# Kernel tuning notes

Measured on AMD Instinct MI355X. Metric: run time of the kernel, lower is better.

## Reference

```python
import jax, jax.numpy as jnp
import numpy as np

B, T, S, H, E, V, M = 64, 59, 32, 512, 300, 34004, 1024  # batch, dec steps, enc len, hidden, embed, vocab, enc dim (bi)


def setup_inputs() -> dict:
    key = jax.random.key(0)
    ks = jax.random.split(key, 14)
    w = lambda k, sh, sc=0.05: jax.random.normal(k, sh, jnp.float32) * sc
    return dict(
        dec_input=jax.random.randint(ks[0], (B, T), 0, V),
        enc_output=w(ks[1], (B, S, M), 1.0),
        enc_h=w(ks[2], (B, H), 1.0),
        enc_c=w(ks[3], (B, H), 1.0),
        embedding=w(ks[4], (V, E)),
        Wx=w(ks[5], (E + H, 4 * H)),   # LSTM input kernel (input = [emb; prev_attention])
        Uh=w(ks[6], (H, 4 * H)),       # LSTM recurrent kernel
        b=jnp.zeros((4 * H,), jnp.float32),
        Wm=w(ks[7], (M, H)),           # Bahdanau memory layer
        Wq=w(ks[8], (H, H)),           # Bahdanau query layer
        v=w(ks[9], (H,)),              # Bahdanau attention vector
        Wa=w(ks[10], (H + M, H)),      # attention_layer (Dense, no bias)
        Wf=w(ks[11], (H, V)),          # output projection to vocab
        bf=jnp.zeros((V,), jnp.float32),
    )


def reference(dec_input, enc_output, enc_h, enc_c, embedding, Wx, Uh, b, Wm, Wq, v, Wa, Wf, bf):
    # Precompute attention keys once: [B,S,H]
    keys = jnp.einsum('bsm,mh->bsh', enc_output, Wm)
    emb = embedding[dec_input]            # [B,T,E] teacher-forced inputs
    emb_t = jnp.swapaxes(emb, 0, 1)       # [T,B,E]

    def step(carry, x_t):
        h, c, attn = carry
        x = jnp.concatenate([x_t, attn], axis=-1)          # [B,E+H]
        z = x @ Wx + h @ Uh + b                            # [B,4H]
        i, f, g, o = jnp.split(z, 4, axis=-1)              # keras gate order i,f,c,o
        c2 = jax.nn.sigmoid(f) * c + jax.nn.sigmoid(i) * jnp.tanh(g)
        h2 = jax.nn.sigmoid(o) * jnp.tanh(c2)
        # Bahdanau attention: score = v . tanh(keys + Wq q)
        q = h2 @ Wq                                        # [B,H]
        scores = jnp.einsum('h,bsh->bs', v, jnp.tanh(keys + q[:, None, :]))
        align = jax.nn.softmax(scores, axis=-1)            # full memory (seq_len == S)
        ctx = jnp.einsum('bs,bsm->bm', align, enc_output)  # [B,M]
        attn2 = jnp.concatenate([h2, ctx], axis=-1) @ Wa   # attention_layer, [B,H]
        logits = attn2 @ Wf + bf                           # [B,V]
        return (h2, c2, attn2), logits

    init = (enc_h, enc_c, jnp.zeros((B, H), enc_h.dtype))
    _, logits = jax.lax.scan(step, init, emb_t)            # [T,B,V]
    return jnp.swapaxes(logits, 0, 1)                      # [B,T,V]
```

## Files before the change

kernel.cpp:

```cpp
#include <hip/hip_runtime.h>
#include <hip/hip_bf16.h>
#include <hip/hip_fp16.h>
#include <cstdint>
#include <cstddef>

typedef unsigned short u16;
typedef unsigned long long u64;
typedef short s8v __attribute__((ext_vector_type(8)));
typedef float f4v __attribute__((ext_vector_type(4)));
typedef _Float16 f16x2 __attribute__((ext_vector_type(2)));

#define DI __device__ __forceinline__

#if defined(__has_builtin)
#  if __has_builtin(__builtin_amdgcn_fdot2)
#    define HAS_FDOT2 1
#  endif
#endif

DI u16 f2bf(float f){ unsigned u = __float_as_uint(f); u += 0x7fffu + ((u>>16)&1u); return (u16)(u>>16); }
DI float bf2f(u16 h){ return __uint_as_float(((unsigned)h)<<16); }
DI int ocol(int pc){ return ((pc>>3)&3)*512 + (pc>>5)*8 + (pc&7); }
DI int ocol2(int s){ int pc = (s & ~31) | ((s&3)<<3) | ((s>>2)&7); return ocol(pc); }
DI int pc2slot(int pc){ return (pc & ~31) | ((pc&7)<<2) | ((pc>>3)&3); }
DI float sigm(float x){ x = fminf(fmaxf(x,-30.f),30.f); return 1.f/(1.f+__expf(-x)); }
DI float tanhx(float x){ x = fminf(fmaxf(x,-15.f),15.f); float e = __expf(-2.f*x); return (1.f-e)/(1.f+e); }
DI uint4 packh8(const u16* h){
  uint4 r; r.x=(unsigned)h[0]|((unsigned)h[1]<<16); r.y=(unsigned)h[2]|((unsigned)h[3]<<16);
  r.z=(unsigned)h[4]|((unsigned)h[5]<<16); r.w=(unsigned)h[6]|((unsigned)h[7]<<16); return r;
}
DI s8v u4s8(uint4 u){ union{uint4 a; s8v b;} t; t.a=u; return t.b; }

DI float qdot(unsigned w, f16x2 hv, float acc){
#ifdef HAS_FDOT2
  f16x2 wv; __builtin_memcpy(&wv, &w, 4);
  return __builtin_amdgcn_fdot2(wv, hv, acc, false);
#else
  __half2 hp = *reinterpret_cast<const __half2*>(&w);
  return acc + (float)hv[0]*__half2float(hp.x) + (float)hv[1]*__half2float(hp.y);
#endif
}

DI unsigned cohld32(const void* p){
  return __hip_atomic_load((const unsigned*)p, __ATOMIC_RELAXED, __HIP_MEMORY_SCOPE_AGENT);
}
DI u64 cohld64(const void* p){
  return __hip_atomic_load((const u64*)p, __ATOMIC_RELAXED, __HIP_MEMORY_SCOPE_AGENT);
}
DI f4v cohldf4(const float* p){
  u64 lo = cohld64(p);
  u64 hi = cohld64(p + 2);
  f4v r;
  r[0]=__uint_as_float((unsigned)lo); r[1]=__uint_as_float((unsigned)(lo>>32));
  r[2]=__uint_as_float((unsigned)hi); r[3]=__uint_as_float((unsigned)(hi>>32));
  return r;
}
DI void cohst32(void* p, unsigned v){
  __hip_atomic_store((unsigned*)p, v, __ATOMIC_RELAXED, __HIP_MEMORY_SCOPE_AGENT);
}
DI void cohst64(void* p, u64 v){
  __hip_atomic_store((u64*)p, v, __ATOMIC_RELAXED, __HIP_MEMORY_SCOPE_AGENT);
}

__global__ __launch_bounds__(256) void k_build(
    const float* __restrict__ bb, const float* __restrict__ eh, const float* __restrict__ ec,
    const int* __restrict__ dec, const float* __restrict__ enc, const float* __restrict__ emb,
    const float* __restrict__ Wx, const float* __restrict__ Uh, const float* __restrict__ Wm,
    const float* __restrict__ Wq, const float* __restrict__ Wa, const float* __restrict__ Wf,
    float* __restrict__ bp, float* __restrict__ h2X, float* __restrict__ cst,
    float* __restrict__ ctxX, unsigned* __restrict__ flags,
    u16* __restrict__ hhi, u16* __restrict__ hlo, u16* __restrict__ encB,
    u16* __restrict__ wq2, u16* __restrict__ wmT, u16* __restrict__ waT,
    u16* __restrict__ wxtpT, u16* __restrict__ wxaT, u16* __restrict__ buhT,
    u16* __restrict__ waA, u16* __restrict__ embB, u16* __restrict__ WfT){
  __shared__ u16 T[64*72];
  int lb = blockIdx.x, tid = threadIdx.x;
  if (lb < 638){
    int i = lb*256 + tid;
    if (i < 2048) bp[i] = bb[ocol2(i)];
    else if (i < 2048+32768) h2X[i-2048] = eh[i-2048];
    else if (i < 2048+65536) cst[i-34816] = ec[i-34816];
    else if (i < 2048+131072) ctxX[i-67584] = 0.f;
    else if (i < 2048+131072+30208) flags[i-133120] = 0u;
  } else if (lb < 1022){
    int i = (lb-638)*256 + tid; if (i >= 64*1536) return;
    int c = i % 1536;
    float f = (c < 512) ? eh[(i/1536)*512 + c] : 0.f;
    u16 hi = f2bf(f);
    hhi[i] = hi;
    hlo[i] = (c < 512) ? f2bf(f - bf2f(hi)) : (u16)0;
  } else if (lb < 2046){
    int g = (lb-1022)*256 + tid; if (g >= 262144) return;
    const float4* p = (const float4*)(enc + (size_t)g*8);
    float4 a = p[0], b = p[1];
    u16 h[8] = {f2bf(a.x),f2bf(a.y),f2bf(a.z),f2bf(a.w),f2bf(b.x),f2bf(b.y),f2bf(b.z),f2bf(b.w)};
    *(uint4*)&encB[(size_t)g*8] = packh8(h);
  } else if (lb < 3070){
    int g = (lb-2046)*256 + tid; if (g >= 262144) return;
    int h = g>>9, c = g&511;
    __half hf = __float2half(Wq[g]);
    wq2[(size_t)(h>>1)*1024 + (c<<1) + (h&1)] = *reinterpret_cast<u16*>(&hf);
  } else if (lb < 3326){
    int g = (lb-3070)*256 + tid; if (g >= 512*128) return;
    int hcol = g/128, o = g%128;
    u16 h[8];
    #pragma unroll
    for(int j=0;j<8;++j){ int m = o*8+j; h[j]=f2bf(Wm[(size_t)m*512 + hcol]); }
    *(uint4*)&wmT[(size_t)hcol*1024 + o*8] = packh8(h);
  } else if (lb < 3710){
    int g = (lb-3326)*256 + tid; if (g >= 512*192) return;
    int c = g/192, o = g%192;
    u16 h[8];
    #pragma unroll
    for(int j=0;j<8;++j){ int k = o*8+j; h[j]=f2bf(Wa[(size_t)k*512 + c]); }
    *(uint4*)&waT[(size_t)c*1536 + o*8] = packh8(h);
  } else if (lb < 4030){
    int g = (lb-3710)*256 + tid; if (g >= 2048*40) return;
    int pc = g/40, o = g%40; int oc = ocol2(pc);
    u16 h[8];
    #pragma unroll
    for(int j=0;j<8;++j){ int e = o*8+j; float f = (e<300)? Wx[(size_t)e*2048 + oc] : 0.f; h[j]=f2bf(f); }
    *(uint4*)&wxtpT[(size_t)pc*320 + o*8] = packh8(h);
  } else if (lb < 5566){
    int g = (lb-4030)*256 + tid; if (g >= 2048*192) return;
    int pc = g/192, o = g%192; int oc = ocol(pc);
    u16 h[8];
    #pragma unroll
    for(int j=0;j<8;++j){
      int kp = o*8+j; int seg = kp>>9; int jd = kp&511;
      float f = Wx[(size_t)(300+jd)*2048 + oc];
      u16 hi = f2bf(f);
      h[j] = (seg==2) ? f2bf(f - bf2f(hi)) : hi;
    }
    *(uint4*)&wxaT[(size_t)pc*1536 + o*8] = packh8(h);
  } else if (lb < 6590){
    int g = (lb-5566)*256 + tid; if (g >= 2048*128) return;
    int pc = g/128, o = g%128; int oc = ocol(pc);
    u16 h[8];
    #pragma unroll
    for(int j=0;j<8;++j){
      int kp = o*8+j; int r = kp&511;
      float f = Uh[(size_t)r*2048 + oc];
      u16 hi = f2bf(f);
      h[j] = (kp<512) ? hi : f2bf(f - bf2f(hi));
    }
    *(uint4*)&buhT[(size_t)pc*1024 + o*8] = packh8(h);
  } else if (lb < 7742){
    int g = (lb-6590)*256 + tid; if (g >= 1536*192) return;
    int r = g/192, o = g%192;
    u16 h[8];
    #pragma unroll
    for(int j=0;j<8;++j){
      int kp = o*8+j; int seg = kp>>9; int jd = kp&511;
      float f = Wa[(size_t)r*512 + jd];
      u16 hi = f2bf(f);
      h[j] = (seg==1) ? f2bf(f - bf2f(hi)) : hi;
    }
    *(uint4*)&waA[(size_t)r*1536 + o*8] = packh8(h);
  } else if (lb < 8332){
    int g = (lb-7742)*256 + tid; if (g >= 3776*40) return;
    int row = g/40, o = g%40;
    int b = row & 63, t = row >> 6;
    int tok = dec[b*59 + t];
    u16 h[8];
    #pragma unroll
    for(int j=0;j<8;++j){ int k = o*8+j; float f = (k<300)? emb[(size_t)tok*300 + k] : 0.f; h[j]=f2bf(f); }
    *(uint4*)&embB[(size_t)row*320 + o*8] = packh8(h);
  } else {
    int lb2 = lb - 8332;
    int n0 = (lb2 % 532)*64, k0 = (lb2/532)*64;
    int kl = tid>>2, nq = (tid&3)*16;
    u16 h[16];
    if (n0 + 64 <= 34004){
      const float4* p = (const float4*)(Wf + (size_t)(k0+kl)*34004 + n0 + nq);
      #pragma unroll
      for(int q=0;q<4;++q){ float4 f = p[q]; h[q*4+0]=f2bf(f.x); h[q*4+1]=f2bf(f.y); h[q*4+2]=f2bf(f.z); h[q*4+3]=f2bf(f.w); }
    } else {
      #pragma unroll
      for(int j=0;j<16;++j){ int n = n0+nq+j; float f = (n<34004)? Wf[(size_t)(k0+kl)*34004 + n] : 0.f; h[j]=f2bf(f); }
    }
    *(uint4*)&T[kl*72 + nq] = packh8(h);
    *(uint4*)&T[kl*72 + nq + 8] = packh8(h+8);
    __syncthreads();
    int nl = tid>>2, kq = (tid&3)*16;
    int n = n0 + nl;
    if (n < 34004){
      u16 o[16];
      #pragma unroll
      for(int j=0;j<16;++j) o[j] = T[(kq+j)*72 + nl];
      *(uint4*)&WfT[(size_t)n*512 + k0 + kq]     = packh8(o);
      *(uint4*)&WfT[(size_t)n*512 + k0 + kq + 8] = packh8(o+8);
    }
  }
}

__global__ void k_wzcT(const float* __restrict__ wzcT, const float* __restrict__ Uh, u16* __restrict__ dst){
  int g = blockIdx.x*256 + threadIdx.x; if (g >= 2048*384) return;
  int pc = g/384, o = g%384; int oc = ocol(pc);
  u16 h[8];
  #pragma unroll
  for(int j=0;j<8;++j){
    int kp = o*8+j; int r = kp % 1536;
    float f = wzcT[(size_t)pc*1536 + r] + ((r<512) ? Uh[(size_t)r*2048 + oc] : 0.f);
    u16 hi = f2bf(f);
    h[j] = (kp<1536) ? hi : f2bf(f - bf2f(hi));
  }
  *(uint4*)&dst[(size_t)pc*3072 + o*8] = packh8(h);
}

__global__ void k_a2dump(const float* __restrict__ h2X, const float* __restrict__ ctxX, u16* __restrict__ dst){
  int g = blockIdx.x*256 + threadIdx.x; if (g >= 3776*192) return;
  int r = g/192, o = g%192;
  u16 h[8];
  #pragma unroll
  for(int j=0;j<8;++j){
    int k = o*8+j;
    float f = (k<512) ? h2X[(size_t)(r+64)*512 + k] : ctxX[(size_t)(r+64)*1024 + (k-512)];
    h[j] = f2bf(f);
  }
  *(uint4*)&dst[(size_t)r*1536 + o*8] = packh8(h);
}

template<int EPI>
DI void gemm_dev(int bx, int by, u16* LSbuf,
    const u16* __restrict__ A, const u16* __restrict__ Bt,
    int M, int N, int K,
    float* __restrict__ Cf, u16* __restrict__ Cb,
    const float* __restrict__ bias, float* __restrict__ Cout){
  u16* Als = LSbuf;
  u16* Bls = LSbuf + 128*40;
  int tid = threadIdx.x;
  int c0 = bx*128, r0 = by*128;
  int wid = tid>>6, wr = wid>>1, wc = wid&1;
  int l15 = tid&15, l4 = (tid>>4)&3;
  f4v acc[4][4];
  #pragma unroll
  for(int m=0;m<4;++m)
  #pragma unroll
  for(int n=0;n<4;++n)
  #pragma unroll
  for(int i=0;i<4;++i) acc[m][n][i] = 0.f;

  int r = tid>>1, hf = tid&1;
  size_t arow = (size_t)min(r0 + r, M-1);
  size_t brow = (size_t)min(c0 + r, N-1);
  const u16* abase = A  + arow*K + hf*16;
  const u16* bbase = Bt + brow*K + hf*16;
  int nk = K >> 5;
  uint4 a0 = ((const uint4*)abase)[0], a1 = ((const uint4*)abase)[1];
  uint4 b0 = ((const uint4*)bbase)[0], b1 = ((const uint4*)bbase)[1];
  for (int ch=0; ch<nk; ++ch){
    __syncthreads();
    *(uint4*)&Als[r*40 + hf*16]     = a0;
    *(uint4*)&Als[r*40 + hf*16 + 8] = a1;
    *(uint4*)&Bls[r*40 + hf*16]     = b0;
    *(uint4*)&Bls[r*40 + hf*16 + 8] = b1;
    __syncthreads();
    if (ch+1 < nk){
      const uint4* ap = (const uint4*)(abase + (ch+1)*32);
      const uint4* bp = (const uint4*)(bbase + (ch+1)*32);
      a0 = ap[0]; a1 = ap[1]; b0 = bp[0]; b1 = bp[1];
    }
    s8v af[4], bfr[4];
    #pragma unroll
    for(int m=0;m<4;++m) af[m]  = *(const s8v*)&Als[(wr*64 + m*16 + l15)*40 + l4*8];
    #pragma unroll
    for(int n=0;n<4;++n) bfr[n] = *(const s8v*)&Bls[(wc*64 + n*16 + l15)*40 + l4*8];
    #pragma unroll
    for(int m=0;m<4;++m)
    #pragma unroll
    for(int n=0;n<4;++n)
      acc[m][n] = __builtin_amdgcn_mfma_f32_16x16x32_bf16(af[m], bfr[n], acc[m][n], 0,0,0);
  }
  __syncthreads();
  float* eps = ((float*)LSbuf) + wid*1024;
  #pragma unroll
  for(int m=0;m<4;++m){
    #pragma unroll
    for(int n=0;n<4;++n)
    #pragma unroll
    for(int i=0;i<4;++i)
      eps[(l4*4 + i)*64 + n*16 + l15] = acc[m][n][i];
    #pragma unroll
    for(int q=0;q<4;++q){
      int row = l4 + q*4;
      f4v v = *(const f4v*)&eps[row*64 + l15*4];
      int gr = r0 + wr*64 + m*16 + row;
      int gc = c0 + wc*64 + l15*4;
      if (gr < M && gc < N){
        if constexpr (EPI==0){
          *(f4v*)&Cf[(size_t)gr*N + gc] = v;
        } else if constexpr (EPI==1){
          f4v bv = *(const f4v*)&bias[gc];
          v += bv;
          *(f4v*)&Cf[(size_t)gr*N + gc] = v;
        } else if constexpr (EPI==2){
          unsigned p0 = ((unsigned)f2bf(v[1])<<16) | f2bf(v[0]);
          unsigned p1 = ((unsigned)f2bf(v[3])<<16) | f2bf(v[2]);
          uint2 pk; pk.x = p0; pk.y = p1;
          *(uint2*)&Cb[(size_t)gr*N + gc] = pk;
        } else {
          f4v bv = *(const f4v*)&bias[gc];
          v += bv;
          int b_ = gr&63, tt = gr>>6;
          *(f4v*)&Cout[((size_t)(b_*59 + tt))*34004 + gc] = v;
        }
      }
    }
  }
}

template<int EPI>
__global__ __launch_bounds__(256,2) void gemm_bf16(
    const u16* __restrict__ A, const u16* __restrict__ Bt,
    int M, int N, int K,
    float* __restrict__ Cf, u16* __restrict__ Cb,
    const float* __restrict__ bias, float* __restrict__ Cout){
  __shared__ u16 LSbuf[2*128*40];
  gemm_dev<EPI>(blockIdx.x, blockIdx.y, LSbuf, A, Bt, M, N, K, Cf, Cb, bias, Cout);
}

__global__ __launch_bounds__(256,2) void k_gemm3(
    const u16* __restrict__ embB, const u16* __restrict__ wxtpT, float* __restrict__ Zemb,
    const float* __restrict__ bp,
    const u16* __restrict__ encB, const u16* __restrict__ wmT, float* __restrict__ keys,
    const u16* __restrict__ wxaT, const u16* __restrict__ waA, float* __restrict__ wzc){
  __shared__ u16 LSbuf[2*128*40];
  int b = blockIdx.x;
  if (b < 480){
    gemm_dev<1>(b%16, b/16, LSbuf, embB, wxtpT, 3776, 2048, 320, Zemb, nullptr, bp, nullptr);
  } else if (b < 544){
    int b2 = b-480;
    gemm_dev<0>(b2%4, b2/4, LSbuf, encB, wmT, 2048, 512, 1024, keys, nullptr, nullptr, nullptr);
  } else {
    int b3 = b-544;
    gemm_dev<0>(b3%12, b3/12, LSbuf, wxaT, waA, 2048, 1536, 1536, wzc, nullptr, nullptr, nullptr);
  }
}

__global__ __launch_bounds__(512,4) void step_fused(
    int t,
    const u16* __restrict__ wzT, const u16* __restrict__ buhT,
    u16* __restrict__ hhi, u16* __restrict__ hlo,
    float* __restrict__ zparts, const float* __restrict__ Zemb,
    float* __restrict__ cst, float* __restrict__ h2X, float* __restrict__ ctxX,
    const u16* __restrict__ wq2, const float* __restrict__ keys,
    const u16* __restrict__ encB, const float* __restrict__ vv,
    unsigned* __restrict__ flags){
  __shared__ float smem[16384];
  int bid = blockIdx.x, tid = threadIdx.x;
  unsigned* flg = flags + (size_t)t*512;
  int variant = (t==0) ? 0 : 1;

  if (bid < 256){
    int sl = bid>>6, cg = bid&63;
    int pc0 = cg*32;
    int wv = tid>>6, lane = tid&63;
    int l15 = lane&15, l4 = lane>>4;
    const u16* Bt = variant ? wzT : buhT;
    int physK = variant ? 3072 : 1024;
    int CS = variant ? 36 : 12;
    int ck0 = sl*CS, ck1 = ck0 + CS;

    f4v acc[4][2];
    #pragma unroll
    for(int m=0;m<4;++m)
    #pragma unroll
    for(int n=0;n<2;++n)
    #pragma unroll
    for(int i=0;i<4;++i) acc[m][n][i] = 0.f;

    for (int c = ck0 + wv; c < ck1; c += 8){
      int k1 = c*32;
      const u16* ap; int inner, kB;
      if (variant==0){
        inner = k1 & 511;
        ap = ((((k1>>9)&3)==1) ? hlo : hhi);
        kB = (k1 < 1024) ? (k1 & 511) : (k1 - 512);
      } else {
        int sg = k1/1536; inner = k1 - sg*1536;
        ap = (sg==1) ? hlo : hhi;
        kB = (k1 < 3072) ? (k1 % 1536) : (1536 + (k1 - 3072));
      }
      uint4 av[4], bv[2];
      #pragma unroll
      for(int m=0;m<4;++m)
        av[m] = *(const uint4*)(ap + (size_t)(m*16 + l15)*1536 + inner + l4*8);
      #pragma unroll
      for(int n=0;n<2;++n)
        bv[n] = *(const uint4*)(Bt + (size_t)(pc0 + n*16 + l15)*physK + kB + l4*8);
      #pragma unroll
      for(int m=0;m<4;++m){
        s8v am = u4s8(av[m]);
        #pragma unroll
        for(int n=0;n<2;++n)
          acc[m][n] = __builtin_amdgcn_mfma_f32_16x16x32_bf16(am, u4s8(bv[n]), acc[m][n], 0,0,0);
      }
    }
    float* red = smem + wv*2048;
    #pragma unroll
    for(int m=0;m<4;++m)
    #pragma unroll
    for(int n=0;n<2;++n)
    #pragma unroll
    for(int i=0;i<4;++i)
      red[(m*16 + l4*4 + i)*32 + n*16 + l15] = acc[m][n][i];
    __syncthreads();

    int rr = tid>>3, cq = (tid&7)*4;
    f4v s = *(const f4v*)&smem[rr*32 + cq];
    #pragma unroll
    for(int w=1;w<8;++w)
      s += *(const f4v*)&smem[w*2048 + rr*32 + cq];
    float* zp = zparts + (size_t)sl*131072 + (size_t)rr*2048 + pc0 + cq;
    cohst64(&zp[0], (u64)__float_as_uint(s[0]) | ((u64)__float_as_uint(s[1])<<32));
    cohst64(&zp[2], (u64)__float_as_uint(s[2]) | ((u64)__float_as_uint(s[3])<<32));
    asm volatile("s_waitcnt vmcnt(0)" ::: "memory");
    __syncthreads();
    if (tid==0) cohst32(&flg[bid], 1u);

  } else {
    int b = bid - 256;
    int j = tid;
    int base = (j>>3)*32 + (j&7)*4;
    f4v ze = *(const f4v*)&Zemb[(size_t)t*131072 + (size_t)b*2048 + base];
    float cprev = cst[(size_t)b*512 + j];
    float vvj = vv[j];
    if (b == 0){
      if (tid < 256){
        while (cohld32(&flg[tid]) == 0u) __builtin_amdgcn_s_sleep(2);
      }
      __syncthreads();
      if (tid==0) cohst32(&flg[511], 1u);
    } else {
      if (tid==0){
        while (cohld32(&flg[511]) == 0u) __builtin_amdgcn_s_sleep(1);
      }
      __syncthreads();
    }
    asm volatile("" ::: "memory");

    float* zl  = smem;
    float* h2s = smem + 2048;
    float* vs2 = smem + 2560;
    float* qs  = smem + 3072;
    float* qpl = smem + 3584;
    float* scl = smem + 7680;
    float* alw = smem + 7712;
    {
      int p4 = tid*4;
      f4v z0; z0[0]=0.f; z0[1]=0.f; z0[2]=0.f; z0[3]=0.f;
      #pragma unroll
      for(int s2=0; s2<4; ++s2)
        z0 += cohldf4(&zparts[(size_t)s2*131072 + (size_t)b*2048 + p4]);
      #pragma unroll
      for(int e=0;e<4;++e)
        zl[pc2slot(p4+e)] = z0[e];
    }
    __syncthreads();
    {
      f4v s4 = ze + *(const f4v*)&zl[base];
      float c2 = sigm(s4[1])*cprev + sigm(s4[0])*tanhx(s4[2]);
      float h2 = sigm(s4[3])*tanhx(c2);
      cst[(size_t)b*512 + j] = c2;
      h2X[(size_t)(t+1)*32768 + (size_t)b*512 + j] = h2;
      h2s[j] = h2; vs2[j] = vvj;
      u16 hh2 = f2bf(h2);
      hhi[(size_t)b*1536 + j] = hh2;
      hlo[(size_t)b*1536 + j] = f2bf(h2 - bf2f(hh2));
    }
    __syncthreads();
    {
      int c8 = (tid&63)*8, hs = tid>>6;
      float qp[8] = {0,0,0,0,0,0,0,0};
      const u16* wp = wq2 + (size_t)(hs*32)*1024 + c8*2;
      #pragma unroll 4
      for(int i=0;i<32;++i){
        int hp = hs*32 + i;
        f16x2 hv; hv[0] = (_Float16)h2s[2*hp]; hv[1] = (_Float16)h2s[2*hp+1];
        uint4 w0 = *(const uint4*)wp;
        uint4 w1 = *(const uint4*)(wp + 8);
        wp += 1024;
        qp[0]=qdot(w0.x,hv,qp[0]); qp[1]=qdot(w0.y,hv,qp[1]);
        qp[2]=qdot(w0.z,hv,qp[2]); qp[3]=qdot(w0.w,hv,qp[3]);
        qp[4]=qdot(w1.x,hv,qp[4]); qp[5]=qdot(w1.y,hv,qp[5]);
        qp[6]=qdot(w1.z,hv,qp[6]); qp[7]=qdot(w1.w,hv,qp[7]);
      }
      *(float4*)&qpl[hs*512 + c8]     = make_float4(qp[0],qp[1],qp[2],qp[3]);
      *(float4*)&qpl[hs*512 + c8 + 4] = make_float4(qp[4],qp[5],qp[6],qp[7]);
    }
    __syncthreads();
    { float s = 0.f; for(int hs=0; hs<8; ++hs) s += qpl[hs*512 + tid]; qs[tid] = s; }
    __syncthreads();
    {
      int s = tid>>4, hh = tid&15;
      const float4* kb4 = (const float4*)(keys + ((size_t)(b*32 + s))*512 + hh*32);
      float part = 0.f;
      #pragma unroll
      for(int i8=0;i8<8;++i8){
        float4 kv = kb4[i8];
        int h = hh*32 + i8*4;
        part += vs2[h+0]*tanhx(kv.x + qs[h+0]);
        part += vs2[h+1]*tanhx(kv.y + qs[h+1]);
        part += vs2[h+2]*tanhx(kv.z + qs[h+2]);
        part += vs2[h+3]*tanhx(kv.w + qs[h+3]);
      }
      #pragma unroll
      for(int m=1;m<16;m<<=1) part += __shfl_xor(part, m, 64);
      if (hh==0) scl[s] = part;
    }
    __syncthreads();
    if (tid < 32){
      float sc = scl[tid];
      float mx = sc;
      #pragma unroll
      for(int m=1;m<32;m<<=1) mx = fmaxf(mx, __shfl_xor(mx, m, 64));
      float e = __expf(sc - mx);
      float sm = e;
      #pragma unroll
      for(int m=1;m<32;m<<=1) sm += __shfl_xor(sm, m, 64);
      alw[tid] = e/sm;
    }
    __syncthreads();
    {
      const u16* eb = encB + (size_t)b*32768;
      int cc = tid*2;
      float c0 = 0.f, c1 = 0.f;
      for(int s=0;s<32;++s){
        float al = alw[s];
        unsigned ev = *(const unsigned*)&eb[(size_t)s*1024 + cc];
        c0 += al*bf2f((u16)(ev&0xffffu));
        c1 += al*bf2f((u16)(ev>>16));
      }
      float2 co; co.x = c0; co.y = c1;
      *(float2*)&ctxX[(size_t)(t+1)*65536 + (size_t)b*1024 + cc] = co;
      u16 x0 = f2bf(c0), x1 = f2bf(c1);
      *(unsigned*)&hhi[(size_t)b*1536 + 512 + cc] = (unsigned)x0 | ((unsigned)x1<<16);
      u16 y0 = f2bf(c0 - bf2f(x0)), y1 = f2bf(c1 - bf2f(x1));
      *(unsigned*)&hlo[(size_t)b*1536 + 512 + cc] = (unsigned)y0 | ((unsigned)y1<<16);
    }
  }
}

extern "C" void kernel_launch(void* const* d_in, const int* in_sizes, int n_in,
                              void* d_out, int out_size, void* d_ws, size_t ws_size,
                              hipStream_t stream){
  const int*   dec = (const int*)d_in[0];
  const float* enc = (const float*)d_in[1];
  const float* eh  = (const float*)d_in[2];
  const float* ec  = (const float*)d_in[3];
  const float* emb = (const float*)d_in[4];
  const float* Wx  = (const float*)d_in[5];
  const float* Uh  = (const float*)d_in[6];
  const float* bb  = (const float*)d_in[7];
  const float* Wm  = (const float*)d_in[8];
  const float* Wq  = (const float*)d_in[9];
  const float* vv  = (const float*)d_in[10];
  const float* Wa  = (const float*)d_in[11];
  const float* Wf  = (const float*)d_in[12];
  const float* bf  = (const float*)d_in[13];
  float* out = (float*)d_out;

  char* w = (char*)d_ws; size_t off = 0;
  auto alloc = [&](size_t bytes)->char*{ char* p = w + off; off = (off + bytes + 255) & ~(size_t)255; return p; };
  u16* WfT   = (u16*)alloc((size_t)34004*512*2);
  u16* attn2 = (u16*)alloc((size_t)3776*512*2);
  size_t liveEnd = off;
  const size_t needB = (size_t)131<<20;
  bool fits = (ws_size >= liveEnd + needB);
  char* wb = fits ? (w + liveEnd) : (char*)d_out;
  size_t offb = 0;
  auto allocB = [&](size_t bytes)->char*{ char* p = wb + offb; offb = (offb + bytes + 255) & ~(size_t)255; return p; };

  u16* wzT   = (u16*)allocB((size_t)2048*3072*2);
  u16* buhT  = (u16*)allocB((size_t)2048*1024*2);
  u16* wq2   = (u16*)allocB((size_t)512*512*2);
  u16* waT   = (u16*)allocB((size_t)512*1536*2);
  u16* wmT   = (u16*)allocB((size_t)512*1024*2);
  u16* wxtpT = (u16*)allocB((size_t)2048*320*2);
  u16* wxaT  = (u16*)allocB((size_t)2048*1536*2);
  u16* waA   = (u16*)allocB((size_t)1536*1536*2);
  float* wzc = (float*)allocB((size_t)2048*1536*4);
  u16* embB  = (u16*)allocB((size_t)3776*320*2);
  u16* encB  = (u16*)allocB((size_t)2048*1024*2);
  float* Zemb  = (float*)allocB((size_t)3776*2048*4);
  float* keys  = (float*)allocB((size_t)2048*512*4);
  float* zparts= (float*)allocB((size_t)9*64*2048*4);
  float* h2X   = (float*)allocB((size_t)60*64*512*4);
  float* ctxX  = (float*)allocB((size_t)60*64*1024*4);
  float* cst   = (float*)allocB((size_t)64*512*4);
  float* bp    = (float*)allocB((size_t)2048*4);
  u16* A2c   = (u16*)allocB((size_t)3776*1536*2);
  u16* hhi   = (u16*)allocB((size_t)64*1536*2);
  u16* hlo   = (u16*)allocB((size_t)64*1536*2);
  unsigned* flags = (unsigned*)allocB((size_t)59*512*4);

  k_build<<<12588,256,0,stream>>>(bb, eh, ec, dec, enc, emb, Wx, Uh, Wm, Wq, Wa, Wf,
                                  bp, h2X, cst, ctxX, flags,
                                  hhi, hlo, encB, wq2, wmT, waT,
                                  wxtpT, wxaT, buhT, waA, embB, WfT);

  k_gemm3<<<736,256,0,stream>>>(embB, wxtpT, Zemb, bp, encB, wmT, keys, wxaT, waA, wzc);
  k_wzcT<<<(2048*384+255)/256,256,0,stream>>>(wzc, Uh, wzT);

  for (int t=0; t<59; ++t){
    step_fused<<<320,512,0,stream>>>(t, wzT, buhT, hhi, hlo, zparts, Zemb,
                                     cst, h2X, ctxX, wq2, keys, encB, vv, flags);
  }

  k_a2dump<<<(3776*192+255)/256,256,0,stream>>>(h2X, ctxX, A2c);
  gemm_bf16<2><<<dim3(4,30),256,0,stream>>>(A2c, waT, 3776, 512, 1536, nullptr, attn2, nullptr, nullptr);
  gemm_bf16<3><<<dim3(266,30),256,0,stream>>>(attn2, WfT, 3776, 34004, 512, nullptr, nullptr, bf, out);
}
```

Measured before the change: 1.720 ms.

## Overlap attention and vocab projection GEMMs with recurrent steps via extra blocks

```diff
diff --git a/kernel.cpp b/kernel.cpp
--- a/kernel.cpp
+++ b/kernel.cpp
@@ -208,19 +208,6 @@
   *(uint4*)&dst[(size_t)pc*3072 + o*8] = packh8(h);
 }
 
-__global__ void k_a2dump(const float* __restrict__ h2X, const float* __restrict__ ctxX, u16* __restrict__ dst){
-  int g = blockIdx.x*256 + threadIdx.x; if (g >= 3776*192) return;
-  int r = g/192, o = g%192;
-  u16 h[8];
-  #pragma unroll
-  for(int j=0;j<8;++j){
-    int k = o*8+j;
-    float f = (k<512) ? h2X[(size_t)(r+64)*512 + k] : ctxX[(size_t)(r+64)*1024 + (k-512)];
-    h[j] = f2bf(f);
-  }
-  *(uint4*)&dst[(size_t)r*1536 + o*8] = packh8(h);
-}
-
 template<int EPI>
 DI void gemm_dev(int bx, int by, u16* LSbuf,
     const u16* __restrict__ A, const u16* __restrict__ Bt,
@@ -338,6 +325,84 @@
   }
 }
 
+template<int OUT>
+DI void wtile(int rb, int cb, float* smem,
+              const u16* __restrict__ A, int K,
+              const u16* __restrict__ Bt, int N,
+              const float* __restrict__ bias, float* __restrict__ Cout,
+              u16* __restrict__ Cb, int ldc){
+  int tid = threadIdx.x;
+  int w = tid>>6, lane = tid&63;
+  int l15 = lane&15, l4 = lane>>4;
+  f4v acc[4][2];
+  #pragma unroll
+  for(int m=0;m<4;++m)
+  #pragma unroll
+  for(int n=0;n<2;++n)
+  #pragma unroll
+  for(int i=0;i<4;++i) acc[m][n][i]=0.f;
+  int c0w = cb*256 + w*32;
+  int nk = K>>5;
+  for (int ch=0; ch<nk; ++ch){
+    uint4 av[4], bv[2];
+    #pragma unroll
+    for(int m=0;m<4;++m)
+      av[m] = *(const uint4*)(A + (size_t)(rb*64 + m*16 + l15)*K + ch*32 + l4*8);
+    #pragma unroll
+    for(int n=0;n<2;++n){
+      int col = min(c0w + n*16 + l15, N-1);
+      bv[n] = *(const uint4*)(Bt + (size_t)col*K + ch*32 + l4*8);
+    }
+    #pragma unroll
+    for(int m=0;m<4;++m){
+      s8v am = u4s8(av[m]);
+      #pragma unroll
+      for(int n=0;n<2;++n)
+        acc[m][n] = __builtin_amdgcn_mfma_f32_16x16x32_bf16(am, u4s8(bv[n]), acc[m][n], 0,0,0);
+    }
+  }
+  float* eps = smem + w*2048;
+  #pragma unroll
+  for(int m=0;m<4;++m)
+  #pragma unroll
+  for(int n=0;n<2;++n)
+  #pragma unroll
+  for(int i=0;i<4;++i)
+    eps[(m*16 + l4*4 + i)*32 + n*16 + l15] = acc[m][n][i];
+  #pragma unroll
+  for(int r8=0;r8<8;++r8){
+    int row = r8*8 + (lane>>3);
+    int c4 = (lane&7)*4;
+    f4v v = *(const f4v*)&eps[row*32 + c4];
+    int gr = rb*64 + row;
+    int gc = c0w + c4;
+    if constexpr (OUT==0){
+      if (gc < N){
+        v += *(const f4v*)&bias[gc];
+        int b_ = gr&63, tt = gr>>6;
+        *(f4v*)&Cout[((size_t)(b_*59 + tt))*34004 + gc] = v;
+      }
+    } else {
+      unsigned p0 = ((unsigned)f2bf(v[1])<<16) | f2bf(v[0]);
+      unsigned p1 = ((unsigned)f2bf(v[3])<<16) | f2bf(v[2]);
+      uint2 pk; pk.x = p0; pk.y = p1;
+      *(uint2*)&Cb[(size_t)gr*ldc + gc] = pk;
+    }
+  }
+}
+
+__global__ __launch_bounds__(512,4) void k_tail(int phase,
+    const u16* __restrict__ A2c, const u16* __restrict__ waT, u16* __restrict__ attn2,
+    const u16* __restrict__ WfT, const float* __restrict__ bf, float* __restrict__ out){
+  __shared__ float smem[16384];
+  if (phase==0){
+    wtile<1>(58, blockIdx.x, smem, A2c, 1536, waT, 512, nullptr, nullptr, attn2, 512);
+  } else {
+    int rb = 57 + blockIdx.x/133, cb = blockIdx.x%133;
+    wtile<0>(rb, cb, smem, attn2, 512, WfT, 34004, bf, out, nullptr, 0);
+  }
+}
+
 __global__ __launch_bounds__(512,4) void step_fused(
     int t,
     const u16* __restrict__ wzT, const u16* __restrict__ buhT,
@@ -346,7 +411,10 @@
     float* __restrict__ cst, float* __restrict__ h2X, float* __restrict__ ctxX,
     const u16* __restrict__ wq2, const float* __restrict__ keys,
     const u16* __restrict__ encB, const float* __restrict__ vv,
-    unsigned* __restrict__ flags){
+    unsigned* __restrict__ flags,
+    u16* __restrict__ A2c, const u16* __restrict__ waT, u16* __restrict__ attn2,
+    const u16* __restrict__ WfT, const float* __restrict__ bfv, float* __restrict__ out,
+    int dowork){
   __shared__ float smem[16384];
   int bid = blockIdx.x, tid = threadIdx.x;
   unsigned* flg = flags + (size_t)t*512;
@@ -419,7 +487,7 @@
     __syncthreads();
     if (tid==0) cohst32(&flg[bid], 1u);
 
-  } else {
+  } else if (bid < 320){
     int b = bid - 256;
     int j = tid;
     int base = (j>>3)*32 + (j&7)*4;
@@ -468,6 +536,7 @@
       u16 hh2 = f2bf(h2);
       hhi[(size_t)b*1536 + j] = hh2;
       hlo[(size_t)b*1536 + j] = f2bf(h2 - bf2f(hh2));
+      A2c[((size_t)t*64 + b)*1536 + j] = hh2;
     }
     __syncthreads();
     {
@@ -535,12 +604,25 @@
       float2 co; co.x = c0; co.y = c1;
       *(float2*)&ctxX[(size_t)(t+1)*65536 + (size_t)b*1024 + cc] = co;
       u16 x0 = f2bf(c0), x1 = f2bf(c1);
-      *(unsigned*)&hhi[(size_t)b*1536 + 512 + cc] = (unsigned)x0 | ((unsigned)x1<<16);
+      unsigned px = (unsigned)x0 | ((unsigned)x1<<16);
+      *(unsigned*)&hhi[(size_t)b*1536 + 512 + cc] = px;
+      *(unsigned*)&A2c[((size_t)t*64 + b)*1536 + 512 + cc] = px;
       u16 y0 = f2bf(c0 - bf2f(x0)), y1 = f2bf(c1 - bf2f(x1));
       *(unsigned*)&hlo[(size_t)b*1536 + 512 + cc] = (unsigned)y0 | ((unsigned)y1<<16);
     }
-  }
-}
+
+  } else if (dowork){
+    int wk = bid - 320;
+    if (wk < 2){
+      if (t >= 1)
+        wtile<1>(t-1, wk, smem, A2c, 1536, waT, 512, nullptr, nullptr, attn2, 512);
+    } else {
+      if (t >= 2)
+        wtile<0>(t-2, wk-2, smem, attn2, 512, WfT, 34004, bfv, out, nullptr, 0);
+    }
+  }
+}
+
 
 extern "C" void kernel_launch(void* const* d_in, const int* in_sizes, int n_in,
                               void* d_out, int out_size, void* d_ws, size_t ws_size,
@@ -565,6 +647,7 @@
   auto alloc = [&](size_t bytes)->char*{ char* p = w + off; off = (off + bytes + 255) & ~(size_t)255; return p; };
   u16* WfT   = (u16*)alloc((size_t)34004*512*2);
   u16* attn2 = (u16*)alloc((size_t)3776*512*2);
+  u16* waT   = (u16*)alloc((size_t)512*1536*2);
   size_t liveEnd = off;
   const size_t needB = (size_t)131<<20;
   bool fits = (ws_size >= liveEnd + needB);
@@ -575,7 +658,6 @@
   u16* wzT   = (u16*)allocB((size_t)2048*3072*2);
   u16* buhT  = (u16*)allocB((size_t)2048*1024*2);
   u16* wq2   = (u16*)allocB((size_t)512*512*2);
-  u16* waT   = (u16*)allocB((size_t)512*1536*2);
   u16* wmT   = (u16*)allocB((size_t)512*1024*2);
   u16* wxtpT = (u16*)allocB((size_t)2048*320*2);
   u16* wxaT  = (u16*)allocB((size_t)2048*1536*2);
@@ -603,12 +685,18 @@
   k_gemm3<<<736,256,0,stream>>>(embB, wxtpT, Zemb, bp, encB, wmT, keys, wxaT, waA, wzc);
   k_wzcT<<<(2048*384+255)/256,256,0,stream>>>(wzc, Uh, wzT);
 
+  int dowork = fits ? 1 : 0;
   for (int t=0; t<59; ++t){
-    step_fused<<<320,512,0,stream>>>(t, wzT, buhT, hhi, hlo, zparts, Zemb,
-                                     cst, h2X, ctxX, wq2, keys, encB, vv, flags);
-  }
-
-  k_a2dump<<<(3776*192+255)/256,256,0,stream>>>(h2X, ctxX, A2c);
-  gemm_bf16<2><<<dim3(4,30),256,0,stream>>>(A2c, waT, 3776, 512, 1536, nullptr, attn2, nullptr, nullptr);
-  gemm_bf16<3><<<dim3(266,30),256,0,stream>>>(attn2, WfT, 3776, 34004, 512, nullptr, nullptr, bf, out);
-}
+    step_fused<<<455,512,0,stream>>>(t, wzT, buhT, hhi, hlo, zparts, Zemb,
+                                     cst, h2X, ctxX, wq2, keys, encB, vv, flags,
+                                     A2c, waT, attn2, WfT, bf, out, dowork);
+  }
+
+  if (fits){
+    k_tail<<<2,512,0,stream>>>(0, A2c, waT, attn2, WfT, bf, out);
+    k_tail<<<266,512,0,stream>>>(1, A2c, waT, attn2, WfT, bf, out);
+  } else {
+    gemm_bf16<2><<<dim3(4,30),256,0,stream>>>(A2c, waT, 3776, 512, 1536, nullptr, attn2, nullptr, nullptr);
+    gemm_bf16<3><<<dim3(266,30),256,0,stream>>>(attn2, WfT, 3776, 34004, 512, nullptr, nullptr, bf, out);
+  }
+}
```

Result: slower. 4.439 ms (+158.1%).
